# Optimization experiments

Measured on AMD Instinct MI355X. Metric: run time of the kernel, lower is better.

Reference implementation:

```python
import jax, jax.numpy as jnp
import numpy as np
from jax import lax

Q = 4          # decimation factor
N_ORDER = 8    # IIR filter order (scipy decimate default / explicit n=8)
RP = 0.05      # passband ripple in dB used by scipy.signal.decimate


def _cheby1_ba(N, rp, Wn):
    """Chebyshev type-I lowpass design, identical math to scipy.signal.cheby1."""
    eps = np.sqrt(10.0 ** (0.1 * rp) - 1.0)
    mu = np.arcsinh(1.0 / eps) / N
    k = np.arange(1, N + 1)
    theta = np.pi * (2 * k - 1) / (2 * N)
    # analog prototype poles (cheb1ap)
    p = -np.sinh(mu) * np.sin(theta) + 1j * np.cosh(mu) * np.cos(theta)
    g = np.prod(-p).real
    if N % 2 == 0:
        g /= np.sqrt(1.0 + eps ** 2)
    # frequency pre-warp (iirfilter with fs=2.0)
    fs = 2.0
    warped = 2.0 * fs * np.tan(np.pi * Wn / fs)
    # lp2lp_zpk
    p = p * warped
    g = g * warped ** N
    # bilinear_zpk
    fs2 = 2.0 * fs
    pd = (fs2 + p) / (fs2 - p)
    zd = -np.ones(N)  # N zeros at z=-1
    gd = g * np.real(1.0 / np.prod(fs2 - p))
    b = np.real(gd * np.poly(zd))
    a = np.real(np.poly(pd))
    return b, a


def _lfilter_zi(b, a):
    """Steady-state initial conditions, identical math to scipy.signal.lfilter_zi."""
    n = len(a)
    comp = np.zeros((n - 1, n - 1))
    comp[0, :] = -a[1:] / a[0]
    comp[1:, :-1] = np.eye(n - 2)
    IminusA = np.eye(n - 1) - comp.T
    B = b[1:] - a[1:] * b[0]
    return np.linalg.solve(IminusA, B)


_B_NP, _A_NP = _cheby1_ba(N_ORDER, RP, 0.8 / Q)
_ZI_NP = _lfilter_zi(_B_NP, _A_NP)


def _lfilter(b, a, x, zi):
    """IIR filter, direct-form II transposed. x: (T, M), zi: (order, M)."""
    def step(z, xt):
        yt = b[0] * xt + z[0]                       # (M,)
        z = jnp.concatenate([z[1:], jnp.zeros_like(z[:1])], axis=0) \
            + b[1:, None] * xt[None, :] - a[1:, None] * yt[None, :]
        return z, yt
    _, y = lax.scan(step, zi, x)
    return y


def _filtfilt(b, a, zi, x):
    """scipy.signal.filtfilt with padtype='odd', padlen=3*max(len(a),len(b)). x: (T, M)."""
    edge = 3 * b.shape[0]  # 27 for an order-8 filter
    left = 2.0 * x[0] - x[edge:0:-1]            # odd extension, left
    right = 2.0 * x[-1] - x[-2:-(edge + 2):-1]  # odd extension, right
    ext = jnp.concatenate([left, x, right], axis=0)
    y = _lfilter(b, a, ext, zi[:, None] * ext[0][None, :])          # forward pass
    y = _lfilter(b, a, y[::-1], zi[:, None] * y[-1][None, :])[::-1]  # backward pass
    return y[edge:-edge]


def _decimate(x):
    """scipy.signal.decimate(x, q=Q, n=8, ftype='iir', axis=-1, zero_phase=True)."""
    B_, C_, T = x.shape
    b = jnp.asarray(_B_NP, x.dtype)
    a = jnp.asarray(_A_NP, x.dtype)
    zi = jnp.asarray(_ZI_NP, x.dtype)
    xt = x.reshape(B_ * C_, T).T  # (T, M) -- time leading for lax.scan
    y = _filtfilt(b, a, zi, xt)
    y = y.T.reshape(B_, C_, T)
    return y[..., ::Q]


def setup_inputs() -> dict:
    key = jax.random.key(0)
    x = jax.random.normal(key, (32, 16, 65536), dtype=jnp.float32)
    return {"x": x}


def reference(x):
    return _decimate(x)
```

## Files before the change

kernel.cpp:

```cpp
#include <hip/hip_runtime.h>
#include <cmath>
#include <complex>

namespace {

constexpr int TLEN   = 65536;
constexpr int NCH    = 512;
constexpr int LEXT   = TLEN + 54;
constexpr int CHUNK  = 256;
constexpr int NCHUNK = 257;
constexpr int PAD    = 4;
constexpr int ROWS4  = 16408;
constexpr size_t BUF_FLOATS = (size_t)ROWS4 * 2048;


struct Coefs {
  float b0,b1,b2,b3,b4,b5,b6,b7,b8;
  float na1,na2,na3,na4,na5,na6,na7,na8;
  float zi0,zi1,zi2,zi3,zi4,zi5,zi6,zi7;
};

#define IIR_STEP(xv, yv)                                  \
  do {                                                    \
    yv = fmaf(cf.b0, (xv), z0);                           \
    z0 = fmaf(cf.na1, yv, fmaf(cf.b1, (xv), z1));         \
    z1 = fmaf(cf.na2, yv, fmaf(cf.b2, (xv), z2));         \
    z2 = fmaf(cf.na3, yv, fmaf(cf.b3, (xv), z3));         \
    z3 = fmaf(cf.na4, yv, fmaf(cf.b4, (xv), z4));         \
    z4 = fmaf(cf.na5, yv, fmaf(cf.b5, (xv), z5));         \
    z5 = fmaf(cf.na6, yv, fmaf(cf.b6, (xv), z6));         \
    z6 = fmaf(cf.na7, yv, fmaf(cf.b7, (xv), z7));         \
    z7 = fmaf(cf.na8, yv, cf.b8 * (xv));                  \
  } while (0)

__global__ __launch_bounds__(256) void k_transpose(const float* __restrict__ x,
                                                   float* __restrict__ ext) {
  __shared__ float lds[64][65];
  const int bt = blockIdx.x;
  const int bm = blockIdx.y;
  const int tid = threadIdx.x;
  const int t0 = bt * 64, m0 = bm * 64;
  {
    const int tl4 = (tid & 15) * 4;
    const int ch0 = tid >> 4;
#pragma unroll
    for (int i = 0; i < 4; ++i) {
      int ch = ch0 + i * 16;
      float4 v = *reinterpret_cast<const float4*>(x + (size_t)(m0 + ch) * TLEN + t0 + tl4);
      lds[ch][tl4 + 0] = v.x; lds[ch][tl4 + 1] = v.y;
      lds[ch][tl4 + 2] = v.z; lds[ch][tl4 + 3] = v.w;
    }
  }
  __syncthreads();
  {
    const int ch = tid & 63;
    const int kk = tid >> 6;
    const int gm = m0 + ch;
#pragma unroll
    for (int i = 0; i < 4; ++i) {
      int gl = 8 + kk + i * 4;
      int g = 16 * bt + gl;
      if (gl <= 22) {
        int tl = 4 * gl - 31;
        float4 v = make_float4(lds[ch][tl], lds[ch][tl + 1], lds[ch][tl + 2], lds[ch][tl + 3]);
        *reinterpret_cast<float4*>(ext + (size_t)g * 2048 + (size_t)gm * 4) = v;
      } else {
        float* base = ext + (size_t)g * 2048 + (size_t)gm * 4;
        base[0] = lds[ch][61]; base[1] = lds[ch][62]; base[2] = lds[ch][63];
        ext[(size_t)(16 * bt + 7) * 2048 + (size_t)gm * 4 + 3] = lds[ch][0];
      }
    }
  }
}

__global__ void k_edges(const float* __restrict__ x, float* __restrict__ ext) {
  const int r = blockIdx.x;
  const int m = threadIdx.x;
  int e, src;
  float base;
  if (r < 27) {
    e = r; src = 27 - r;
    base = x[(size_t)m * TLEN];
  } else {
    int j = r - 27;
    e = TLEN + 27 + j; src = TLEN - 2 - j;
    base = x[(size_t)m * TLEN + (TLEN - 1)];
  }
  float v = 2.0f * base - x[(size_t)m * TLEN + src];
  int s = e + PAD;
  ext[(size_t)(s >> 2) * 2048 + (size_t)m * 4 + (s & 3)] = v;
}

__global__ __launch_bounds__(256) void k_fwd(const float* __restrict__ ext,
                                             float* __restrict__ yb, Coefs cf) {
  const int m = blockIdx.y * 256 + threadIdx.x;
  const int c = blockIdx.x;
  float z0, z1, z2, z3, z4, z5, z6, z7;
  const int e0 = (c == 0) ? 0 : 256 * (c - 1);
  const int s4_begin = (e0 + PAD) >> 2;
  {
    float x0 = ext[(size_t)s4_begin * 2048 + (size_t)m * 4];
    z0 = cf.zi0 * x0; z1 = cf.zi1 * x0; z2 = cf.zi2 * x0; z3 = cf.zi3 * x0;
    z4 = cf.zi4 * x0; z5 = cf.zi5 * x0; z6 = cf.zi6 * x0; z7 = cf.zi7 * x0;
  }
  const int store_s4 = 64 * c + 1;
  const int s4_last = min(64 * c + 64, 16398);
  const float4* xv = reinterpret_cast<const float4*>(ext);
  float4* yv = reinterpret_cast<float4*>(yb);
  float4 b0 = xv[(size_t)(s4_begin + 0) * 512 + m];
  float4 b1 = xv[(size_t)(s4_begin + 1) * 512 + m];
  float4 b2 = xv[(size_t)(s4_begin + 2) * 512 + m];
  float4 b3 = xv[(size_t)(s4_begin + 3) * 512 + m];
  for (int g = s4_begin; g <= s4_last; g += 4) {
    float4 c0 = b0, c1 = b1, c2 = b2, c3 = b3;
    b0 = xv[(size_t)(g + 4) * 512 + m];
    b1 = xv[(size_t)(g + 5) * 512 + m];
    b2 = xv[(size_t)(g + 6) * 512 + m];
    b3 = xv[(size_t)(g + 7) * 512 + m];
#pragma unroll
    for (int j = 0; j < 4; ++j) {
      float4 xq = (j == 0) ? c0 : (j == 1) ? c1 : (j == 2) ? c2 : c3;
      const int sg = g + j;
      float4 o;
      IIR_STEP(xq.x, o.x);
      IIR_STEP(xq.y, o.y);
      IIR_STEP(xq.z, o.z);
      IIR_STEP(xq.w, o.w);
      if (sg >= store_s4 && sg <= s4_last)
        yv[(size_t)sg * 512 + m] = o;
    }
  }
}

__global__ __launch_bounds__(256) void k_bwd(const float* __restrict__ yb,
                                             float* __restrict__ ot, Coefs cf) {
  const int m = blockIdx.y * 256 + threadIdx.x;
  const int c = blockIdx.x;
  const int uend = min(256 * (c + 1), LEXT) - 1;
  const int own_lo = 256 * c;
  float z0, z1, z2, z3, z4, z5, z6, z7;
  const int ustart = (c <= 1) ? 0 : (256 * c - 258);
  {
    int sI = 65593 - ustart;
    float y0 = yb[(size_t)(sI >> 2) * 2048 + (size_t)m * 4 + (sI & 3)];
    z0 = cf.zi0 * y0; z1 = cf.zi1 * y0; z2 = cf.zi2 * y0; z3 = cf.zi3 * y0;
    z4 = cf.zi4 * y0; z5 = cf.zi5 * y0; z6 = cf.zi6 * y0; z7 = cf.zi7 * y0;
  }
  int g_begin;
  if (c <= 1) {
#pragma unroll
    for (int s = 65593; s >= 65592; --s) {
      float yin = yb[(size_t)(s >> 2) * 2048 + (size_t)m * 4 + (s & 3)];
      float wv; IIR_STEP(yin, wv);
      (void)wv;
    }
    g_begin = 16397;
  } else {
    g_begin = (65593 - ustart) >> 2;
  }
  const int g_stop = (c <= 255) ? (16334 - 64 * c) : 1;
  const float4* yv = reinterpret_cast<const float4*>(yb);
  auto ld = [&](int r) {
    int rr = r < 0 ? 0 : r;
    return yv[(size_t)rr * 512 + m];
  };
  float4 b0 = ld(g_begin), b1 = ld(g_begin - 1), b2 = ld(g_begin - 2), b3 = ld(g_begin - 3);
  for (int g = g_begin; g >= g_stop; g -= 4) {
    float4 c0 = b0, c1 = b1, c2 = b2, c3 = b3;
    b0 = ld(g - 4); b1 = ld(g - 5); b2 = ld(g - 6); b3 = ld(g - 7);
#pragma unroll
    for (int j = 0; j < 4; ++j) {
      const int sg = g - j;
      float4 q = (j == 0) ? c0 : (j == 1) ? c1 : (j == 2) ? c2 : c3;
      float w3, w2, w1, w0;
      IIR_STEP(q.w, w3);
      IIR_STEP(q.z, w2);
      IIR_STEP(q.y, w1);
      IIR_STEP(q.x, w0);
      (void)w2; (void)w1; (void)w0;
      const int u3 = 65590 - 4 * sg;
      const int n = sg - 7;
      if (u3 >= own_lo && u3 <= uend && n >= 0 && n < 16384)
        ot[(size_t)n * 512 + m] = w3;
    }
  }
}

__global__ __launch_bounds__(256) void k_outT(const float* __restrict__ ot,
                                              float* __restrict__ out) {
  __shared__ float lds[64][65];
  const int bn = blockIdx.x;
  const int bm = blockIdx.y;
  const int tid = threadIdx.x;
  const int n0 = bn * 64, m0 = bm * 64;
  {
    const int ml4 = (tid & 15) * 4;
    const int nl0 = tid >> 4;
#pragma unroll
    for (int i = 0; i < 4; ++i) {
      int nl = nl0 + i * 16;
      float4 v = *reinterpret_cast<const float4*>(ot + (size_t)(n0 + nl) * 512 + m0 + ml4);
      lds[ml4 + 0][nl] = v.x; lds[ml4 + 1][nl] = v.y;
      lds[ml4 + 2][nl] = v.z; lds[ml4 + 3][nl] = v.w;
    }
  }
  __syncthreads();
  {
    const int nl4 = (tid & 15) * 4;
    const int ml0 = tid >> 4;
#pragma unroll
    for (int i = 0; i < 4; ++i) {
      int ml = ml0 + i * 16;
      float4 v = make_float4(lds[ml][nl4], lds[ml][nl4 + 1], lds[ml][nl4 + 2], lds[ml][nl4 + 3]);
      *reinterpret_cast<float4*>(out + (size_t)(m0 + ml) * 16384 + n0 + nl4) = v;
    }
  }
}

static void solve8(double Mm[8][9], double* zi) {
  for (int col = 0; col < 8; ++col) {
    int piv = col;
    for (int r = col + 1; r < 8; ++r)
      if (std::fabs(Mm[r][col]) > std::fabs(Mm[piv][col])) piv = r;
    if (piv != col)
      for (int j = 0; j < 9; ++j) { double t = Mm[col][j]; Mm[col][j] = Mm[piv][j]; Mm[piv][j] = t; }
    double d = Mm[col][col];
    for (int j = col; j < 9; ++j) Mm[col][j] /= d;
    for (int r = 0; r < 8; ++r)
      if (r != col) {
        double f = Mm[r][col];
        if (f != 0.0)
          for (int j = col; j < 9; ++j) Mm[r][j] -= f * Mm[col][j];
      }
  }
  for (int i = 0; i < 8; ++i) zi[i] = Mm[i][8];
}

static Coefs make_coefs() {
  using cd = std::complex<double>;
  const int N = 8;
  const double rp = 0.05, Wn = 0.8 / 4.0;
  double eps = std::sqrt(std::pow(10.0, 0.1 * rp) - 1.0);
  double mu = std::asinh(1.0 / eps) / N;
  cd p[8];
  for (int i = 0; i < N; ++i) {
    double th = M_PI * (2.0 * (i + 1) - 1.0) / (2.0 * N);
    p[i] = cd(-std::sinh(mu) * std::sin(th), std::cosh(mu) * std::cos(th));
  }
  cd pr(1.0, 0.0);
  for (int i = 0; i < N; ++i) pr *= -p[i];
  double g = pr.real();
  g /= std::sqrt(1.0 + eps * eps);
  const double fs = 2.0;
  double warped = 2.0 * fs * std::tan(M_PI * Wn / fs);
  for (int i = 0; i < N; ++i) p[i] *= warped;
  g *= std::pow(warped, (double)N);
  const double fs2 = 2.0 * fs;
  cd pd[8], dpr(1.0, 0.0);
  for (int i = 0; i < N; ++i) {
    pd[i] = (cd(fs2, 0.0) + p[i]) / (cd(fs2, 0.0) - p[i]);
    dpr *= (cd(fs2, 0.0) - p[i]);
  }
  double gd = g * (cd(1.0, 0.0) / dpr).real();
  static const double binom[9] = {1, 8, 28, 56, 70, 56, 28, 8, 1};
  double b[9], a[9];
  for (int i = 0; i < 9; ++i) b[i] = gd * binom[i];
  cd cp[9]; cp[0] = cd(1, 0);
  for (int i = 1; i < 9; ++i) cp[i] = cd(0, 0);
  for (int i = 0; i < N; ++i)
    for (int j = i + 1; j >= 1; --j) cp[j] -= pd[i] * cp[j - 1];
  for (int i = 0; i < 9; ++i) a[i] = cp[i].real();
  double Mm[8][9];
  for (int i = 0; i < 8; ++i) {
    for (int j = 0; j < 9; ++j) Mm[i][j] = 0.0;
    Mm[i][0] += a[i + 1];
    Mm[i][i] += 1.0;
    if (i < 7) Mm[i][i + 1] = -1.0;
    Mm[i][8] = b[i + 1] - a[i + 1] * b[0];
  }
  double zi[8];
  solve8(Mm, zi);
  Coefs cf;
  cf.b0 = (float)b[0]; cf.b1 = (float)b[1]; cf.b2 = (float)b[2]; cf.b3 = (float)b[3];
  cf.b4 = (float)b[4]; cf.b5 = (float)b[5]; cf.b6 = (float)b[6]; cf.b7 = (float)b[7];
  cf.b8 = (float)b[8];
  cf.na1 = (float)(-a[1]); cf.na2 = (float)(-a[2]); cf.na3 = (float)(-a[3]);
  cf.na4 = (float)(-a[4]); cf.na5 = (float)(-a[5]); cf.na6 = (float)(-a[6]);
  cf.na7 = (float)(-a[7]); cf.na8 = (float)(-a[8]);
  cf.zi0 = (float)zi[0]; cf.zi1 = (float)zi[1]; cf.zi2 = (float)zi[2]; cf.zi3 = (float)zi[3];
  cf.zi4 = (float)zi[4]; cf.zi5 = (float)zi[5]; cf.zi6 = (float)zi[6]; cf.zi7 = (float)zi[7];
  return cf;
}

}

extern "C" void kernel_launch(void* const* d_in, const int* in_sizes, int n_in,
                              void* d_out, int out_size, void* d_ws, size_t ws_size,
                              hipStream_t stream) {
  (void)in_sizes; (void)n_in; (void)out_size; (void)ws_size;
  const float* x = (const float*)d_in[0];
  float* out = (float*)d_out;
  float* ext = (float*)d_ws;
  float* yb  = ext + BUF_FLOATS;
  float* ot  = ext;
  Coefs cf = make_coefs();
  hipLaunchKernelGGL(k_transpose, dim3(TLEN / 64, NCH / 64), dim3(256), 0, stream, x, ext);
  hipLaunchKernelGGL(k_edges, dim3(54), dim3(512), 0, stream, x, ext);
  hipLaunchKernelGGL(k_fwd, dim3(NCHUNK, 2), dim3(256), 0, stream, ext, yb, cf);
  hipLaunchKernelGGL(k_bwd, dim3(NCHUNK, 2), dim3(256), 0, stream, yb, ot, cf);
  hipLaunchKernelGGL(k_outT, dim3(16384 / 64, NCH / 64), dim3(256), 0, stream, ot, out);
}
```

Before: 341.6 us.

## Realign extended buffer padding for aligned float4 transposes and packed decimated output

Changes the time padding from 4 to 5 so input samples land on float4 boundaries. The transpose kernel can then copy whole 256-sample tiles with aligned vector loads and stores instead of handling misaligned edge words. The backward pass now packs four decimated outputs into one float4 store in an interleaved layout, and the output transpose moves float4 granules through shared memory. Both recursive passes also deepen register prefetch to eight rows. The boundary indexing in the chunked warm-up logic is rewritten, which risks off-by-one errors at the chunk and sequence edges.

```diff
diff --git a/kernel.cpp b/kernel.cpp
--- a/kernel.cpp
+++ b/kernel.cpp
@@ -7,10 +7,9 @@
 constexpr int TLEN   = 65536;
 constexpr int NCH    = 512;
 constexpr int LEXT   = TLEN + 54;
-constexpr int CHUNK  = 256;
 constexpr int NCHUNK = 257;
-constexpr int PAD    = 4;
-constexpr int ROWS4  = 16408;
+constexpr int PAD    = 5;
+constexpr int ROWS4  = 16416;
 constexpr size_t BUF_FLOATS = (size_t)ROWS4 * 2048;
 
 
@@ -35,41 +34,29 @@
 
 __global__ __launch_bounds__(256) void k_transpose(const float* __restrict__ x,
                                                    float* __restrict__ ext) {
-  __shared__ float lds[64][65];
-  const int bt = blockIdx.x;
-  const int bm = blockIdx.y;
+  __shared__ float lds[64 * 260];
+  const int bx = blockIdx.x;
+  const int m0 = blockIdx.y * 64;
   const int tid = threadIdx.x;
-  const int t0 = bt * 64, m0 = bm * 64;
-  {
-    const int tl4 = (tid & 15) * 4;
-    const int ch0 = tid >> 4;
-#pragma unroll
-    for (int i = 0; i < 4; ++i) {
-      int ch = ch0 + i * 16;
-      float4 v = *reinterpret_cast<const float4*>(x + (size_t)(m0 + ch) * TLEN + t0 + tl4);
-      lds[ch][tl4 + 0] = v.x; lds[ch][tl4 + 1] = v.y;
-      lds[ch][tl4 + 2] = v.z; lds[ch][tl4 + 3] = v.w;
-    }
+  const int t0 = bx * 256;
+#pragma unroll
+  for (int i = 0; i < 16; ++i) {
+    int idx = tid + i * 256;
+    int ch = idx >> 6;
+    int tq = idx & 63;
+    float4 v = *reinterpret_cast<const float4*>(
+        x + (size_t)(m0 + ch) * TLEN + t0 + tq * 4);
+    *reinterpret_cast<float4*>(&lds[ch * 260 + tq * 4]) = v;
   }
   __syncthreads();
-  {
-    const int ch = tid & 63;
-    const int kk = tid >> 6;
-    const int gm = m0 + ch;
-#pragma unroll
-    for (int i = 0; i < 4; ++i) {
-      int gl = 8 + kk + i * 4;
-      int g = 16 * bt + gl;
-      if (gl <= 22) {
-        int tl = 4 * gl - 31;
-        float4 v = make_float4(lds[ch][tl], lds[ch][tl + 1], lds[ch][tl + 2], lds[ch][tl + 3]);
-        *reinterpret_cast<float4*>(ext + (size_t)g * 2048 + (size_t)gm * 4) = v;
-      } else {
-        float* base = ext + (size_t)g * 2048 + (size_t)gm * 4;
-        base[0] = lds[ch][61]; base[1] = lds[ch][62]; base[2] = lds[ch][63];
-        ext[(size_t)(16 * bt + 7) * 2048 + (size_t)gm * 4 + 3] = lds[ch][0];
-      }
-    }
+#pragma unroll
+  for (int i = 0; i < 16; ++i) {
+    int idx = tid + i * 256;
+    int j = idx >> 6;
+    int ch = idx & 63;
+    float4 v = *reinterpret_cast<const float4*>(&lds[ch * 260 + j * 4]);
+    *reinterpret_cast<float4*>(
+        ext + (size_t)(64 * bx + 8 + j) * 2048 + (size_t)(m0 + ch) * 4) = v;
   }
 }
 
@@ -96,14 +83,25 @@
   const int m = blockIdx.y * 256 + threadIdx.x;
   const int c = blockIdx.x;
   float z0, z1, z2, z3, z4, z5, z6, z7;
-  const int e0 = (c == 0) ? 0 : 256 * (c - 1);
-  const int s4_begin = (e0 + PAD) >> 2;
-  {
+  int s4_begin, store_s4;
+  if (c == 0) {
+    float x0 = ext[(size_t)1 * 2048 + (size_t)m * 4 + 1];
+    z0 = cf.zi0 * x0; z1 = cf.zi1 * x0; z2 = cf.zi2 * x0; z3 = cf.zi3 * x0;
+    z4 = cf.zi4 * x0; z5 = cf.zi5 * x0; z6 = cf.zi6 * x0; z7 = cf.zi7 * x0;
+#pragma unroll
+    for (int s = 5; s < 8; ++s) {
+      float xin = ext[(size_t)(s >> 2) * 2048 + (size_t)m * 4 + (s & 3)];
+      float yv; IIR_STEP(xin, yv);
+      yb[(size_t)(s >> 2) * 2048 + (size_t)m * 4 + (s & 3)] = yv;
+    }
+    s4_begin = 2; store_s4 = 2;
+  } else {
+    s4_begin = 64 * c - 62;
     float x0 = ext[(size_t)s4_begin * 2048 + (size_t)m * 4];
     z0 = cf.zi0 * x0; z1 = cf.zi1 * x0; z2 = cf.zi2 * x0; z3 = cf.zi3 * x0;
     z4 = cf.zi4 * x0; z5 = cf.zi5 * x0; z6 = cf.zi6 * x0; z7 = cf.zi7 * x0;
-  }
-  const int store_s4 = 64 * c + 1;
+    store_s4 = 64 * c + 1;
+  }
   const int s4_last = min(64 * c + 64, 16398);
   const float4* xv = reinterpret_cast<const float4*>(ext);
   float4* yv = reinterpret_cast<float4*>(yb);
@@ -111,12 +109,17 @@
   float4 b1 = xv[(size_t)(s4_begin + 1) * 512 + m];
   float4 b2 = xv[(size_t)(s4_begin + 2) * 512 + m];
   float4 b3 = xv[(size_t)(s4_begin + 3) * 512 + m];
+  float4 b4 = xv[(size_t)(s4_begin + 4) * 512 + m];
+  float4 b5 = xv[(size_t)(s4_begin + 5) * 512 + m];
+  float4 b6 = xv[(size_t)(s4_begin + 6) * 512 + m];
+  float4 b7 = xv[(size_t)(s4_begin + 7) * 512 + m];
   for (int g = s4_begin; g <= s4_last; g += 4) {
     float4 c0 = b0, c1 = b1, c2 = b2, c3 = b3;
-    b0 = xv[(size_t)(g + 4) * 512 + m];
-    b1 = xv[(size_t)(g + 5) * 512 + m];
-    b2 = xv[(size_t)(g + 6) * 512 + m];
-    b3 = xv[(size_t)(g + 7) * 512 + m];
+    b0 = b4; b1 = b5; b2 = b6; b3 = b7;
+    b4 = xv[(size_t)(g + 8) * 512 + m];
+    b5 = xv[(size_t)(g + 9) * 512 + m];
+    b6 = xv[(size_t)(g + 10) * 512 + m];
+    b7 = xv[(size_t)(g + 11) * 512 + m];
 #pragma unroll
     for (int j = 0; j < 4; ++j) {
       float4 xq = (j == 0) ? c0 : (j == 1) ? c1 : (j == 2) ? c2 : c3;
@@ -133,87 +136,84 @@
 }
 
 __global__ __launch_bounds__(256) void k_bwd(const float* __restrict__ yb,
-                                             float* __restrict__ ot, Coefs cf) {
+                                             float* __restrict__ ot2, Coefs cf) {
   const int m = blockIdx.y * 256 + threadIdx.x;
   const int c = blockIdx.x;
-  const int uend = min(256 * (c + 1), LEXT) - 1;
   const int own_lo = 256 * c;
   float z0, z1, z2, z3, z4, z5, z6, z7;
-  const int ustart = (c <= 1) ? 0 : (256 * c - 258);
-  {
-    int sI = 65593 - ustart;
-    float y0 = yb[(size_t)(sI >> 2) * 2048 + (size_t)m * 4 + (sI & 3)];
+  int g_begin;
+  if (c <= 1) {
+    float y0 = yb[(size_t)16398 * 2048 + (size_t)m * 4 + 2];
     z0 = cf.zi0 * y0; z1 = cf.zi1 * y0; z2 = cf.zi2 * y0; z3 = cf.zi3 * y0;
     z4 = cf.zi4 * y0; z5 = cf.zi5 * y0; z6 = cf.zi6 * y0; z7 = cf.zi7 * y0;
-  }
-  int g_begin;
-  if (c <= 1) {
-#pragma unroll
-    for (int s = 65593; s >= 65592; --s) {
+#pragma unroll
+    for (int s = 65594; s >= 65584; --s) {
       float yin = yb[(size_t)(s >> 2) * 2048 + (size_t)m * 4 + (s & 3)];
       float wv; IIR_STEP(yin, wv);
       (void)wv;
     }
-    g_begin = 16397;
+    g_begin = 16395;
   } else {
-    g_begin = (65593 - ustart) >> 2;
-  }
-  const int g_stop = (c <= 255) ? (16334 - 64 * c) : 1;
+    g_begin = 16463 - 64 * c;
+    float y0 = yb[(size_t)g_begin * 2048 + (size_t)m * 4 + 3];
+    z0 = cf.zi0 * y0; z1 = cf.zi1 * y0; z2 = cf.zi2 * y0; z3 = cf.zi3 * y0;
+    z4 = cf.zi4 * y0; z5 = cf.zi5 * y0; z6 = cf.zi6 * y0; z7 = cf.zi7 * y0;
+  }
+  const int g_stop = max(1, 16334 - 64 * c);
   const float4* yv = reinterpret_cast<const float4*>(yb);
   auto ld = [&](int r) {
     int rr = r < 0 ? 0 : r;
     return yv[(size_t)rr * 512 + m];
   };
   float4 b0 = ld(g_begin), b1 = ld(g_begin - 1), b2 = ld(g_begin - 2), b3 = ld(g_begin - 3);
+  float4 b4 = ld(g_begin - 4), b5 = ld(g_begin - 5), b6 = ld(g_begin - 6), b7 = ld(g_begin - 7);
   for (int g = g_begin; g >= g_stop; g -= 4) {
     float4 c0 = b0, c1 = b1, c2 = b2, c3 = b3;
-    b0 = ld(g - 4); b1 = ld(g - 5); b2 = ld(g - 6); b3 = ld(g - 7);
+    b0 = b4; b1 = b5; b2 = b6; b3 = b7;
+    b4 = ld(g - 8); b5 = ld(g - 9); b6 = ld(g - 10); b7 = ld(g - 11);
+    float4 pack;
 #pragma unroll
     for (int j = 0; j < 4; ++j) {
-      const int sg = g - j;
       float4 q = (j == 0) ? c0 : (j == 1) ? c1 : (j == 2) ? c2 : c3;
       float w3, w2, w1, w0;
       IIR_STEP(q.w, w3);
       IIR_STEP(q.z, w2);
       IIR_STEP(q.y, w1);
       IIR_STEP(q.x, w0);
-      (void)w2; (void)w1; (void)w0;
-      const int u3 = 65590 - 4 * sg;
-      const int n = sg - 7;
-      if (u3 >= own_lo && u3 <= uend && n >= 0 && n < 16384)
-        ot[(size_t)n * 512 + m] = w3;
+      (void)w3; (void)w2; (void)w1;
+      if (j == 0) pack.w = w0;
+      else if (j == 1) pack.z = w0;
+      else if (j == 2) pack.y = w0;
+      else pack.x = w0;
     }
-  }
-}
-
-__global__ __launch_bounds__(256) void k_outT(const float* __restrict__ ot,
+    if (65594 - 4 * g >= own_lo && g >= 11 && g <= 16391)
+      *reinterpret_cast<float4*>(ot2 + (size_t)((g - 11) >> 2) * 2048 + (size_t)m * 4) = pack;
+  }
+}
+
+__global__ __launch_bounds__(256) void k_outT(const float* __restrict__ ot2,
                                               float* __restrict__ out) {
-  __shared__ float lds[64][65];
-  const int bn = blockIdx.x;
-  const int bm = blockIdx.y;
+  __shared__ float4 lds4[64 * 65];
+  const int q0 = blockIdx.x * 64;
+  const int m0 = blockIdx.y * 64;
   const int tid = threadIdx.x;
-  const int n0 = bn * 64, m0 = bm * 64;
-  {
-    const int ml4 = (tid & 15) * 4;
-    const int nl0 = tid >> 4;
-#pragma unroll
-    for (int i = 0; i < 4; ++i) {
-      int nl = nl0 + i * 16;
-      float4 v = *reinterpret_cast<const float4*>(ot + (size_t)(n0 + nl) * 512 + m0 + ml4);
-      lds[ml4 + 0][nl] = v.x; lds[ml4 + 1][nl] = v.y;
-      lds[ml4 + 2][nl] = v.z; lds[ml4 + 3][nl] = v.w;
-    }
+#pragma unroll
+  for (int i = 0; i < 16; ++i) {
+    int idx = tid + i * 256;
+    int ql = idx >> 6;
+    int ml = idx & 63;
+    lds4[ql * 65 + ml] = *reinterpret_cast<const float4*>(
+        ot2 + (size_t)(q0 + ql) * 2048 + (size_t)(m0 + ml) * 4);
   }
   __syncthreads();
-  {
-    const int nl4 = (tid & 15) * 4;
-    const int ml0 = tid >> 4;
-#pragma unroll
-    for (int i = 0; i < 4; ++i) {
-      int ml = ml0 + i * 16;
-      float4 v = make_float4(lds[ml][nl4], lds[ml][nl4 + 1], lds[ml][nl4 + 2], lds[ml][nl4 + 3]);
-      *reinterpret_cast<float4*>(out + (size_t)(m0 + ml) * 16384 + n0 + nl4) = v;
-    }
+#pragma unroll
+  for (int i = 0; i < 16; ++i) {
+    int idx = tid + i * 256;
+    int ml = idx >> 6;
+    int ql = idx & 63;
+    float4 v = lds4[ql * 65 + ml];
+    *reinterpret_cast<float4*>(
+        out + (size_t)(m0 + ml) * 16384 + (size_t)(q0 + ql) * 4) = v;
   }
 }
 
@@ -302,11 +302,11 @@
   float* out = (float*)d_out;
   float* ext = (float*)d_ws;
   float* yb  = ext + BUF_FLOATS;
-  float* ot  = ext;
+  float* ot2 = ext;
   Coefs cf = make_coefs();
-  hipLaunchKernelGGL(k_transpose, dim3(TLEN / 64, NCH / 64), dim3(256), 0, stream, x, ext);
+  hipLaunchKernelGGL(k_transpose, dim3(TLEN / 256, NCH / 64), dim3(256), 0, stream, x, ext);
   hipLaunchKernelGGL(k_edges, dim3(54), dim3(512), 0, stream, x, ext);
   hipLaunchKernelGGL(k_fwd, dim3(NCHUNK, 2), dim3(256), 0, stream, ext, yb, cf);
-  hipLaunchKernelGGL(k_bwd, dim3(NCHUNK, 2), dim3(256), 0, stream, yb, ot, cf);
-  hipLaunchKernelGGL(k_outT, dim3(16384 / 64, NCH / 64), dim3(256), 0, stream, ot, out);
-}
+  hipLaunchKernelGGL(k_bwd, dim3(NCHUNK, 2), dim3(256), 0, stream, yb, ot2, cf);
+  hipLaunchKernelGGL(k_outT, dim3(4096 / 64, NCH / 64), dim3(256), 0, stream, ot2, out);
+}
```

After: 335.2 us. About the same (-1.9%).
